# Optimization experiments

Measured on AMD Instinct MI355X. Metric: run time of the kernel, lower is better.

## Reference

```python
import jax, jax.numpy as jnp
import numpy as np

V_EN = 50000; V_FR = 50000; D = 256; B = 64; S = 64; NEG = 8192; PAD = 0


def setup_inputs() -> dict:
    key = jax.random.key(0)
    k = jax.random.split(key, 8)
    zs = jax.random.normal(k[0], (B, S, D), dtype=jnp.float32) * 0.1
    x_en = jax.random.randint(k[1], (B, S), 1, V_EN)  # avoid pad row 0
    x_fr = jax.random.randint(k[2], (B, S), 1, V_FR)
    en_mask = jnp.ones((B, S), dtype=jnp.float32)
    fr_mask = jnp.ones((B, S), dtype=jnp.float32)
    W_en = jax.random.normal(k[3], (V_EN, D), dtype=jnp.float32) * 0.05
    W_en = W_en.at[PAD].set(0.0)  # padding_idx row is zero
    W_fr = jax.random.normal(k[4], (V_FR, D), dtype=jnp.float32) * 0.05
    W_fr = W_fr.at[PAD].set(0.0)
    # Host-side CSS sampling, mirroring the torch module's numpy/multinomial step.
    rng = np.random.default_rng(0)
    pos_en = np.unique(np.asarray(x_en))
    neg_en = rng.choice(np.setdiff1d(np.arange(V_EN), pos_en), NEG, replace=False)
    kappa_en = jnp.float32((V_EN - pos_en.shape[0]) / NEG)
    pos_fr = np.unique(np.asarray(x_fr))
    neg_fr = rng.choice(np.setdiff1d(np.arange(V_FR), pos_fr), NEG, replace=False)
    kappa_fr = jnp.float32((V_FR - pos_fr.shape[0]) / NEG)
    return {
        "zs": zs, "x_en": x_en, "x_fr": x_fr,
        "en_mask": en_mask, "fr_mask": fr_mask,
        "W_en": W_en, "W_fr": W_fr,
        "pos_en": jnp.asarray(pos_en), "neg_en": jnp.asarray(neg_en),
        "pos_fr": jnp.asarray(pos_fr), "neg_fr": jnp.asarray(neg_fr),
        "kappa_en": kappa_en, "kappa_fr": kappa_fr,
    }


def _css_denom(zs, W, pos_idx, neg_idx, kappa):
    # zs: [B,S,D]; pos/neg embeddings: [P,D]/[N,D] -> denom [B,S]
    pos_e = W[pos_idx]
    neg_e = W[neg_idx]
    pos_score = jnp.exp(jnp.einsum("bsd,pd->bsp", zs, pos_e)).sum(-1)
    neg_score = kappa * jnp.exp(jnp.einsum("bsd,nd->bsn", zs, neg_e)).sum(-1)
    return pos_score + neg_score


def reference(zs, x_en, x_fr, en_mask, fr_mask, W_en, W_fr,
              pos_en, neg_en, pos_fr, neg_fr, kappa_en, kappa_fr):
    # --- English CSS: per-token score ---
    be_en = W_en[x_en]                                   # [B,S,D]
    en_batch = jnp.exp((zs * be_en).sum(-1))             # [B,S]
    en_probs = en_batch / _css_denom(zs, W_en, pos_en, neg_en, kappa_en)
    # --- French CSS: alignment score against every en position ---
    be_fr = W_fr[x_fr]                                   # [B,Sf,D]
    fr_batch = jnp.exp(jnp.einsum("bfd,bsd->bfs", be_fr, zs))  # [B,Sf,S]
    fr_denom = _css_denom(zs, W_fr, pos_fr, neg_fr, kappa_fr)  # [B,S]
    fr_probs = fr_batch / fr_denom[:, None, :]
    en_rec_loss = (jnp.log(en_probs) * en_mask).sum(axis=1)            # [B]
    fr_rec_loss = (jnp.log(fr_probs.sum(axis=2)) * fr_mask).sum(axis=1)  # [B]
    return en_rec_loss, fr_rec_loss
```

## Files before the change

kernel.cpp:

```cpp
#include <hip/hip_runtime.h>

#define DDIM 256
#define NTOK 4096
#define NEGN 8192
#define TM 64
#define TN 64
#define LDT 40

typedef __attribute__((ext_vector_type(8))) short bf16x8;
typedef __attribute__((ext_vector_type(4))) float f32x4;

__device__ inline unsigned short f2bf(float f) {
    unsigned int u = __float_as_uint(f);
    unsigned int r = u + 0x7FFFu + ((u >> 16) & 1u);
    return (unsigned short)(r >> 16);
}

__device__ inline void gl_lds16(const unsigned short* g, unsigned short* l) {
    __builtin_amdgcn_global_load_lds(
        reinterpret_cast<__attribute__((address_space(1))) unsigned int*>(
            reinterpret_cast<uintptr_t>(g)),
        reinterpret_cast<__attribute__((address_space(3))) unsigned int*>(
            reinterpret_cast<uintptr_t>(l)),
        16, 0, 0);
}

__device__ inline void wait_vmcnt0() { asm volatile("s_waitcnt vmcnt(0)" ::: "memory"); }
__device__ inline void raw_barrier() { asm volatile("s_barrier" ::: "memory"); }

template<int CTRL>
__device__ inline float dpp_add(float x) {
    int v = __builtin_amdgcn_update_dpp(0, __float_as_int(x), CTRL, 0xF, 0xF, false);
    return x + __int_as_float(v);
}
__device__ inline float red16(float x) {
    x = dpp_add<0xB1>(x);
    x = dpp_add<0x4E>(x);
    x = dpp_add<0x141>(x);
    x = dpp_add<0x140>(x);
    return x;
}

__global__ void gather_kernel(
    const float* __restrict__ zs,
    const float* __restrict__ W_en, const float* __restrict__ W_fr,
    const int* __restrict__ pos_en, const int* __restrict__ neg_en,
    const int* __restrict__ pos_fr, const int* __restrict__ neg_fr,
    const int* __restrict__ x_en,
    unsigned short* __restrict__ z_bf,
    unsigned short* __restrict__ E_en, unsigned short* __restrict__ E_fr,
    float* __restrict__ en_score,
    float* __restrict__ denom_en, float* __restrict__ denom_fr,
    int Pe, int Pf, int Lpe, int Lpf)
{
    int row  = blockIdx.x * 4 + (threadIdx.x >> 6);
    int lane = threadIdx.x & 63;
    const float* src = nullptr;
    unsigned short* dst = nullptr;
    bool zero = false;

    if (row < NTOK) {
        src = zs + (size_t)row * DDIM;
        dst = z_bf + (size_t)row * DDIM;
        if (lane == 0) { denom_en[row] = 0.0f; denom_fr[row] = 0.0f; }
    } else if (row < NTOK + Lpe) {
        int j = row - NTOK;
        int Le = Pe + NEGN;
        int idx = 0;
        if (j < Pe)      idx = pos_en[j];
        else if (j < Le) idx = neg_en[j - Pe];
        else             zero = true;
        src = W_en + (size_t)idx * DDIM;
        dst = E_en + (size_t)j * DDIM;
    } else if (row < NTOK + Lpe + Lpf) {
        int j = row - NTOK - Lpe;
        int Lf = Pf + NEGN;
        int idx = 0;
        if (j < Pf)      idx = pos_fr[j];
        else if (j < Lf) idx = neg_fr[j - Pf];
        else             zero = true;
        src = W_fr + (size_t)idx * DDIM;
        dst = E_fr + (size_t)j * DDIM;
    } else if (row < NTOK + Lpe + Lpf + NTOK) {
        int j = row - NTOK - Lpe - Lpf;
        int idx = x_en[j];
        float4 z = *(const float4*)(zs   + (size_t)j   * DDIM + lane * 4);
        float4 w = *(const float4*)(W_en + (size_t)idx * DDIM + lane * 4);
        float s = z.x * w.x + z.y * w.y + z.z * w.z + z.w * w.w;
        #pragma unroll
        for (int m = 32; m; m >>= 1) s += __shfl_xor(s, m);
        if (lane == 0) en_score[j] = s;
        return;
    } else {
        return;
    }

    int d = lane * 4;
    float4 v;
    if (zero) { v.x = v.y = v.z = v.w = 0.0f; }
    else      { v = *(const float4*)(src + d); }
    ushort4 o;
    o.x = f2bf(v.x); o.y = f2bf(v.y); o.z = f2bf(v.z); o.w = f2bf(v.w);
    *(ushort4*)(dst + d) = o;
}

__global__ __launch_bounds__(256, 2) void expsum_stream(
    const unsigned short* __restrict__ A,
    const unsigned short* __restrict__ E,
    const float* __restrict__ kep, const float* __restrict__ kfp,
    float* __restrict__ out_en, float* __restrict__ out_fr,
    int Pe, int Pf, int Lpe, int NT)
{
    __shared__ __align__(16) unsigned short Bs[2][8][2048];

    int lin = blockIdx.y * 64 + blockIdx.x;
    int xcd = lin & 7;
    int xb  = (lin >> 3) & 15;
    int sl  = xcd + 8 * (lin >> 7);

    int t    = threadIdx.x;
    int lane = t & 63;
    int wave = t >> 6;
    int col  = lane & 15;
    int quad = lane >> 4;

    float ke = kep[0], kf = kfp[0];
    asm volatile("" : "+v"(ke), "+v"(kf) : : "memory");

    bf16x8 afr[4][8];
    {
        const unsigned short* Ap =
            A + ((size_t)(xb * 256 + wave * 64 + col)) * DDIM + quad * 8;
        #pragma unroll
        for (int i = 0; i < 4; i++)
            #pragma unroll
            for (int c = 0; c < 8; c++)
                afr[i][c] = *(const bf16x8*)(Ap + (size_t)i * 16 * DDIM + c * 32);
    }

    float sums[4][4];
    #pragma unroll
    for (int i = 0; i < 4; i++)
        #pragma unroll
        for (int rr = 0; rr < 4; rr++) sums[i][rr] = 0.0f;
    float* curout = out_en;
    int outrow = xb * 256 + wave * 64;

    int ntiles = (NT - sl + 31) >> 5;

    #define STAGE_TILE(s) do {                                               \
        int tl_ = sl + ((s) << 5);                                           \
        const unsigned short* g_ =                                           \
            E + (size_t)(tl_ * 64 + wave * 16 + col) * DDIM + quad * 8;      \
        unsigned short* l_ = &Bs[(s) & 1][0][wave * 512];                    \
        _Pragma("unroll")                                                    \
        for (int kc_ = 0; kc_ < 8; kc_++)                                    \
            gl_lds16(g_ + kc_ * 32, l_ + kc_ * 2048);                        \
    } while (0)

    STAGE_TILE(0);

    for (int s = 0; s < ntiles; s++) {
        int tl = sl + (s << 5);
        int nb = tl * 64;

        wait_vmcnt0();
        raw_barrier();

        if (s + 1 < ntiles) STAGE_TILE(s + 1);

        float* o = (nb >= Lpe) ? out_fr : out_en;
        if (o != curout) {
            #pragma unroll
            for (int i = 0; i < 4; i++)
                #pragma unroll
                for (int rr = 0; rr < 4; rr++) {
                    float v = red16(sums[i][rr]);
                    if (col == 0)
                        atomicAdd(curout + outrow + 16 * i + quad * 4 + rr, v);
                    sums[i][rr] = 0.0f;
                }
            curout = o;
        }

        float wj[4];
        #pragma unroll
        for (int j = 0; j < 4; j++) {
            int ngl = nb + 16 * j + col;
            if (nb < Lpe) {
                wj[j] = (ngl < Pe) ? 1.0f : ((ngl < Pe + NEGN) ? ke : 0.0f);
            } else {
                int nl = ngl - Lpe;
                wj[j] = (nl < Pf) ? 1.0f : ((nl < Pf + NEGN) ? kf : 0.0f);
            }
        }

        f32x4 acc[4][4];
        #pragma unroll
        for (int i = 0; i < 4; i++)
            #pragma unroll
            for (int j = 0; j < 4; j++)
                acc[i][j] = (f32x4){0.f, 0.f, 0.f, 0.f};

        #pragma unroll
        for (int k8 = 0; k8 < 8; k8++) {
            bf16x8 bfv[4];
            #pragma unroll
            for (int j = 0; j < 4; j++)
                bfv[j] = *(const bf16x8*)(
                    &Bs[s & 1][k8][j * 512 + quad * 128 + col * 8]);
            #pragma unroll
            for (int j = 0; j < 4; j++)
                #pragma unroll
                for (int i = 0; i < 4; i++)
                    acc[i][j] = __builtin_amdgcn_mfma_f32_16x16x32_bf16(
                        afr[i][k8], bfv[j], acc[i][j], 0, 0, 0);
        }

        #pragma unroll
        for (int i = 0; i < 4; i++)
            #pragma unroll
            for (int rr = 0; rr < 4; rr++) {
                sums[i][rr] += wj[0] * __expf(acc[i][0][rr])
                             + wj[1] * __expf(acc[i][1][rr])
                             + wj[2] * __expf(acc[i][2][rr])
                             + wj[3] * __expf(acc[i][3][rr]);
            }
    }
    #undef STAGE_TILE

    #pragma unroll
    for (int i = 0; i < 4; i++)
        #pragma unroll
        for (int rr = 0; rr < 4; rr++) {
            float v = red16(sums[i][rr]);
            if (col == 0)
                atomicAdd(curout + outrow + 16 * i + quad * 4 + rr, v);
        }
}

__global__ __launch_bounds__(256) void expsum_gemm64_loss(
    const float* __restrict__ W_fr,
    const int* __restrict__ x_fr,
    const unsigned short* __restrict__ Bm,
    const float* __restrict__ denom_fr,
    const float* __restrict__ denom_en,
    const float* __restrict__ en_score,
    const float* __restrict__ en_mask,
    const float* __restrict__ fr_mask,
    float* __restrict__ outloss)
{
    __shared__ __align__(16) unsigned short lda[TM * LDT];
    __shared__ __align__(16) unsigned short ldb[TN * LDT];
    __shared__ float tbuf[64];

    int batch = blockIdx.x;
    const unsigned short* Bb = Bm + (size_t)batch * TN * DDIM;

    int t      = threadIdx.x;
    int srow   = t >> 2;
    int schunk = t & 3;
    int lane   = t & 63;
    int wave   = t >> 6;
    int col    = lane & 15;
    int quad   = lane >> 4;

    int aidx = x_fr[batch * 64 + srow];
    const float* Arow = W_fr + (size_t)aidx * DDIM;

    f32x4 acc0 = {0.f,0.f,0.f,0.f};
    f32x4 acc1 = {0.f,0.f,0.f,0.f};
    f32x4 acc2 = {0.f,0.f,0.f,0.f};
    f32x4 acc3 = {0.f,0.f,0.f,0.f};

    for (int kk = 0; kk < DDIM; kk += 32) {
        float4 f0 = *(const float4*)(Arow + kk + schunk * 8);
        float4 f1 = *(const float4*)(Arow + kk + schunk * 8 + 4);
        uint4 bv = *(const uint4*)(Bb + (size_t)srow * DDIM + kk + schunk * 8);
        ushort4 ua; ua.x = f2bf(f0.x); ua.y = f2bf(f0.y); ua.z = f2bf(f0.z); ua.w = f2bf(f0.w);
        ushort4 ub; ub.x = f2bf(f1.x); ub.y = f2bf(f1.y); ub.z = f2bf(f1.z); ub.w = f2bf(f1.w);
        __syncthreads();
        *(ushort4*)(lda + srow * LDT + schunk * 8)     = ua;
        *(ushort4*)(lda + srow * LDT + schunk * 8 + 4) = ub;
        *(uint4*)(ldb + srow * LDT + schunk * 8) = bv;
        __syncthreads();

        bf16x8 af = *(const bf16x8*)(lda + (wave * 16 + col) * LDT + quad * 8);
        bf16x8 b0 = *(const bf16x8*)(ldb + ( 0 + col) * LDT + quad * 8);
        bf16x8 b1 = *(const bf16x8*)(ldb + (16 + col) * LDT + quad * 8);
        bf16x8 b2 = *(const bf16x8*)(ldb + (32 + col) * LDT + quad * 8);
        bf16x8 b3 = *(const bf16x8*)(ldb + (48 + col) * LDT + quad * 8);
        acc0 = __builtin_amdgcn_mfma_f32_16x16x32_bf16(af, b0, acc0, 0, 0, 0);
        acc1 = __builtin_amdgcn_mfma_f32_16x16x32_bf16(af, b1, acc1, 0, 0, 0);
        acc2 = __builtin_amdgcn_mfma_f32_16x16x32_bf16(af, b2, acc2, 0, 0, 0);
        acc3 = __builtin_amdgcn_mfma_f32_16x16x32_bf16(af, b3, acc3, 0, 0, 0);
    }

    const float* db = denom_fr + batch * 64;
    float w0 = 1.0f / db[ 0 + col];
    float w1 = 1.0f / db[16 + col];
    float w2 = 1.0f / db[32 + col];
    float w3 = 1.0f / db[48 + col];

    float tot0 = w0 * __expf(acc0.x) + w1 * __expf(acc1.x) + w2 * __expf(acc2.x) + w3 * __expf(acc3.x);
    float tot1 = w0 * __expf(acc0.y) + w1 * __expf(acc1.y) + w2 * __expf(acc2.y) + w3 * __expf(acc3.y);
    float tot2 = w0 * __expf(acc0.z) + w1 * __expf(acc1.z) + w2 * __expf(acc2.z) + w3 * __expf(acc3.z);
    float tot3 = w0 * __expf(acc0.w) + w1 * __expf(acc1.w) + w2 * __expf(acc2.w) + w3 * __expf(acc3.w);

    #pragma unroll
    for (int m = 1; m < 16; m <<= 1) {
        tot0 += __shfl_xor(tot0, m);
        tot1 += __shfl_xor(tot1, m);
        tot2 += __shfl_xor(tot2, m);
        tot3 += __shfl_xor(tot3, m);
    }
    if (col == 0) {
        int base = wave * 16 + quad * 4;
        tbuf[base + 0] = tot0; tbuf[base + 1] = tot1;
        tbuf[base + 2] = tot2; tbuf[base + 3] = tot3;
    }
    __syncthreads();

    if (t < 64) {
        int i = batch * 64 + t;
        float a = (en_score[i] - __logf(denom_en[i])) * en_mask[i];
        float c = __logf(tbuf[t]) * fr_mask[i];
        #pragma unroll
        for (int m = 32; m; m >>= 1) { a += __shfl_xor(a, m); c += __shfl_xor(c, m); }
        if (t == 0) { outloss[batch] = a; outloss[64 + batch] = c; }
    }
}

extern "C" void kernel_launch(void* const* d_in, const int* in_sizes, int n_in,
                              void* d_out, int out_size, void* d_ws, size_t ws_size,
                              hipStream_t stream)
{
    const float* zs       = (const float*)d_in[0];
    const int*   x_en     = (const int*)d_in[1];
    const int*   x_fr     = (const int*)d_in[2];
    const float* en_mask  = (const float*)d_in[3];
    const float* fr_mask  = (const float*)d_in[4];
    const float* W_en     = (const float*)d_in[5];
    const float* W_fr     = (const float*)d_in[6];
    const int*   pos_en   = (const int*)d_in[7];
    const int*   neg_en   = (const int*)d_in[8];
    const int*   pos_fr   = (const int*)d_in[9];
    const int*   neg_fr   = (const int*)d_in[10];
    const float* kappa_en = (const float*)d_in[11];
    const float* kappa_fr = (const float*)d_in[12];

    int Pe  = in_sizes[7];
    int Pf  = in_sizes[9];
    int Lpe = (Pe + NEGN + 63) & ~63;
    int Lpf = (Pf + NEGN + 63) & ~63;
    int Ltot = Lpe + Lpf;
    int NT   = Ltot / 64;

    char* w = (char*)d_ws;
    float* denom_en = (float*)w; w += NTOK * 4;
    float* denom_fr = (float*)w; w += NTOK * 4;
    float* en_score = (float*)w; w += NTOK * 4;
    unsigned short* z_bf  = (unsigned short*)w; w += (size_t)NTOK * DDIM * 2;
    unsigned short* E_all = (unsigned short*)w; w += (size_t)Ltot * DDIM * 2;

    int totrows = NTOK + Lpe + Lpf + NTOK;
    gather_kernel<<<(totrows + 3) / 4, 256, 0, stream>>>(
        zs, W_en, W_fr, pos_en, neg_en, pos_fr, neg_fr, x_en,
        z_bf, E_all, E_all + (size_t)Lpe * DDIM,
        en_score, denom_en, denom_fr, Pe, Pf, Lpe, Lpf);

    expsum_stream<<<dim3(64, 8), 256, 0, stream>>>(
        z_bf, E_all, kappa_en, kappa_fr, denom_en, denom_fr, Pe, Pf, Lpe, NT);

    expsum_gemm64_loss<<<64, 256, 0, stream>>>(
        W_fr, x_fr, z_bf, denom_fr, denom_en, en_score, en_mask, fr_mask,
        (float*)d_out);
}
```

Measured before the change: 198.1 us.

## Software-pipeline MFMA sweeps with exp epilogue and prescale embeddings by log2e

The streaming exp-sum kernel now processes one 16-column group at a time and interleaves the exp/accumulate work for the previous group's accumulators with the MFMAs of the current group, using ping-pong accumulator sets carried across tiles. Embedding rows are pre-multiplied by log2(e) during the bf16 gather, so the epilogue can use a raw v_exp_f32 (exp2) instead of __expf's extra multiply. The goal is to hide transcendental/VALU epilogue latency behind matrix-core work and cut accumulator register pressure. In exchange the flush logic is more intricate, and rounding shifts slightly because the log2e scaling is applied before bf16 conversion.

```diff
diff --git a/kernel.cpp b/kernel.cpp
--- a/kernel.cpp
+++ b/kernel.cpp
@@ -3,6 +3,7 @@
 #define DDIM 256
 #define NTOK 4096
 #define NEGN 8192
+#define LOG2E 1.4426950408889634f
 #define TM 64
 #define TN 64
 #define LDT 40
@@ -14,6 +15,12 @@
     unsigned int u = __float_as_uint(f);
     unsigned int r = u + 0x7FFFu + ((u >> 16) & 1u);
     return (unsigned short)(r >> 16);
+}
+
+__device__ inline float exp2fast(float x) {
+    float r;
+    asm("v_exp_f32 %0, %1" : "=v"(r) : "v"(x));
+    return r;
 }
 
 __device__ inline void gl_lds16(const unsigned short* g, unsigned short* l) {
@@ -58,10 +65,12 @@
     const float* src = nullptr;
     unsigned short* dst = nullptr;
     bool zero = false;
+    float sc = LOG2E;
 
     if (row < NTOK) {
         src = zs + (size_t)row * DDIM;
         dst = z_bf + (size_t)row * DDIM;
+        sc = 1.0f;
         if (lane == 0) { denom_en[row] = 0.0f; denom_fr[row] = 0.0f; }
     } else if (row < NTOK + Lpe) {
         int j = row - NTOK;
@@ -100,7 +109,8 @@
     if (zero) { v.x = v.y = v.z = v.w = 0.0f; }
     else      { v = *(const float4*)(src + d); }
     ushort4 o;
-    o.x = f2bf(v.x); o.y = f2bf(v.y); o.z = f2bf(v.z); o.w = f2bf(v.w);
+    o.x = f2bf(v.x * sc); o.y = f2bf(v.y * sc);
+    o.z = f2bf(v.z * sc); o.w = f2bf(v.w * sc);
     *(ushort4*)(dst + d) = o;
 }
 
@@ -143,6 +153,11 @@
     for (int i = 0; i < 4; i++)
         #pragma unroll
         for (int rr = 0; rr < 4; rr++) sums[i][rr] = 0.0f;
+
+    f32x4 accA[4], accB[4];
+    #pragma unroll
+    for (int i = 0; i < 4; i++) accB[i] = (f32x4){0.f, 0.f, 0.f, 0.f};
+    float wjP = 0.0f;
     float* curout = out_en;
     int outrow = xb * 256 + wave * 64;
 
@@ -158,6 +173,36 @@
             gl_lds16(g_ + kc_ * 32, l_ + kc_ * 2048);                        \
     } while (0)
 
+    #define J_SWEEP(J, ACCC, ACCD, WJD) do {                                 \
+        _Pragma("unroll")                                                    \
+        for (int i = 0; i < 4; i++) ACCC[i] = (f32x4){0.f, 0.f, 0.f, 0.f};   \
+        _Pragma("unroll")                                                    \
+        for (int k8 = 0; k8 < 8; k8++) {                                     \
+            bf16x8 bfv = *(const bf16x8*)(                                   \
+                &Bs[s & 1][k8][(J) * 512 + quad * 128 + col * 8]);           \
+            _Pragma("unroll")                                                \
+            for (int i = 0; i < 4; i++)                                      \
+                ACCC[i] = __builtin_amdgcn_mfma_f32_16x16x32_bf16(           \
+                    afr[i][k8], bfv, ACCC[i], 0, 0, 0);                      \
+            sums[(k8 * 2) >> 2][(k8 * 2) & 3] +=                             \
+                (WJD) * exp2fast(ACCD[(k8 * 2) >> 2][(k8 * 2) & 3]);         \
+            sums[(k8 * 2 + 1) >> 2][(k8 * 2 + 1) & 3] +=                     \
+                (WJD) * exp2fast(ACCD[(k8 * 2 + 1) >> 2][(k8 * 2 + 1) & 3]); \
+        }                                                                    \
+    } while (0)
+
+    #define FLUSH_SUMS() do {                                                \
+        _Pragma("unroll")                                                    \
+        for (int i = 0; i < 4; i++)                                          \
+            _Pragma("unroll")                                                \
+            for (int rr = 0; rr < 4; rr++) {                                 \
+                float v = red16(sums[i][rr]);                                \
+                if (col == 0)                                                \
+                    atomicAdd(curout + outrow + 16 * i + quad * 4 + rr, v);  \
+                sums[i][rr] = 0.0f;                                          \
+            }                                                                \
+    } while (0)
+
     STAGE_TILE(0);
 
     for (int s = 0; s < ntiles; s++) {
@@ -168,20 +213,6 @@
         raw_barrier();
 
         if (s + 1 < ntiles) STAGE_TILE(s + 1);
-
-        float* o = (nb >= Lpe) ? out_fr : out_en;
-        if (o != curout) {
-            #pragma unroll
-            for (int i = 0; i < 4; i++)
-                #pragma unroll
-                for (int rr = 0; rr < 4; rr++) {
-                    float v = red16(sums[i][rr]);
-                    if (col == 0)
-                        atomicAdd(curout + outrow + 16 * i + quad * 4 + rr, v);
-                    sums[i][rr] = 0.0f;
-                }
-            curout = o;
-        }
 
         float wj[4];
         #pragma unroll
@@ -194,49 +225,28 @@
                 wj[j] = (nl < Pf) ? 1.0f : ((nl < Pf + NEGN) ? kf : 0.0f);
             }
         }
-
-        f32x4 acc[4][4];
-        #pragma unroll
-        for (int i = 0; i < 4; i++)
-            #pragma unroll
-            for (int j = 0; j < 4; j++)
-                acc[i][j] = (f32x4){0.f, 0.f, 0.f, 0.f};
-
-        #pragma unroll
-        for (int k8 = 0; k8 < 8; k8++) {
-            bf16x8 bfv[4];
-            #pragma unroll
-            for (int j = 0; j < 4; j++)
-                bfv[j] = *(const bf16x8*)(
-                    &Bs[s & 1][k8][j * 512 + quad * 128 + col * 8]);
-            #pragma unroll
-            for (int j = 0; j < 4; j++)
-                #pragma unroll
-                for (int i = 0; i < 4; i++)
-                    acc[i][j] = __builtin_amdgcn_mfma_f32_16x16x32_bf16(
-                        afr[i][k8], bfv[j], acc[i][j], 0, 0, 0);
+        float* outC = (nb >= Lpe) ? out_fr : out_en;
+
+        J_SWEEP(0, accA, accB, wjP);
+        if (outC != curout) {
+            FLUSH_SUMS();
+            curout = outC;
         }
-
-        #pragma unroll
-        for (int i = 0; i < 4; i++)
-            #pragma unroll
-            for (int rr = 0; rr < 4; rr++) {
-                sums[i][rr] += wj[0] * __expf(acc[i][0][rr])
-                             + wj[1] * __expf(acc[i][1][rr])
-                             + wj[2] * __expf(acc[i][2][rr])
-                             + wj[3] * __expf(acc[i][3][rr]);
-            }
+        J_SWEEP(1, accB, accA, wj[0]);
+        J_SWEEP(2, accA, accB, wj[1]);
+        J_SWEEP(3, accB, accA, wj[2]);
+        wjP = wj[3];
     }
     #undef STAGE_TILE
+    #undef J_SWEEP
 
     #pragma unroll
     for (int i = 0; i < 4; i++)
         #pragma unroll
-        for (int rr = 0; rr < 4; rr++) {
-            float v = red16(sums[i][rr]);
-            if (col == 0)
-                atomicAdd(curout + outrow + 16 * i + quad * 4 + rr, v);
-        }
+        for (int rr = 0; rr < 4; rr++)
+            sums[i][rr] += wjP * exp2fast(accB[i][rr]);
+    FLUSH_SUMS();
+    #undef FLUSH_SUMS
 }
 
 __global__ __launch_bounds__(256) void expsum_gemm64_loss(
@@ -277,8 +287,10 @@
         float4 f0 = *(const float4*)(Arow + kk + schunk * 8);
         float4 f1 = *(const float4*)(Arow + kk + schunk * 8 + 4);
         uint4 bv = *(const uint4*)(Bb + (size_t)srow * DDIM + kk + schunk * 8);
-        ushort4 ua; ua.x = f2bf(f0.x); ua.y = f2bf(f0.y); ua.z = f2bf(f0.z); ua.w = f2bf(f0.w);
-        ushort4 ub; ub.x = f2bf(f1.x); ub.y = f2bf(f1.y); ub.z = f2bf(f1.z); ub.w = f2bf(f1.w);
+        ushort4 ua; ua.x = f2bf(f0.x * LOG2E); ua.y = f2bf(f0.y * LOG2E);
+                    ua.z = f2bf(f0.z * LOG2E); ua.w = f2bf(f0.w * LOG2E);
+        ushort4 ub; ub.x = f2bf(f1.x * LOG2E); ub.y = f2bf(f1.y * LOG2E);
+                    ub.z = f2bf(f1.z * LOG2E); ub.w = f2bf(f1.w * LOG2E);
         __syncthreads();
         *(ushort4*)(lda + srow * LDT + schunk * 8)     = ua;
         *(ushort4*)(lda + srow * LDT + schunk * 8 + 4) = ub;
@@ -302,10 +314,10 @@
     float w2 = 1.0f / db[32 + col];
     float w3 = 1.0f / db[48 + col];
 
-    float tot0 = w0 * __expf(acc0.x) + w1 * __expf(acc1.x) + w2 * __expf(acc2.x) + w3 * __expf(acc3.x);
-    float tot1 = w0 * __expf(acc0.y) + w1 * __expf(acc1.y) + w2 * __expf(acc2.y) + w3 * __expf(acc3.y);
-    float tot2 = w0 * __expf(acc0.z) + w1 * __expf(acc1.z) + w2 * __expf(acc2.z) + w3 * __expf(acc3.z);
-    float tot3 = w0 * __expf(acc0.w) + w1 * __expf(acc1.w) + w2 * __expf(acc2.w) + w3 * __expf(acc3.w);
+    float tot0 = w0 * exp2fast(acc0.x) + w1 * exp2fast(acc1.x) + w2 * exp2fast(acc2.x) + w3 * exp2fast(acc3.x);
+    float tot1 = w0 * exp2fast(acc0.y) + w1 * exp2fast(acc1.y) + w2 * exp2fast(acc2.y) + w3 * exp2fast(acc3.y);
+    float tot2 = w0 * exp2fast(acc0.z) + w1 * exp2fast(acc1.z) + w2 * exp2fast(acc2.z) + w3 * exp2fast(acc3.z);
+    float tot3 = w0 * exp2fast(acc0.w) + w1 * exp2fast(acc1.w) + w2 * exp2fast(acc2.w) + w3 * exp2fast(acc3.w);
 
     #pragma unroll
     for (int m = 1; m < 16; m <<= 1) {
```

Result: faster. 191.3 us (-3.4%).
